# Kernel optimization log

Measured on AMD Instinct MI355X. Metric: run time of the kernel, lower is better.

Reference implementation:

```python
import jax, jax.numpy as jnp
import numpy as np

N, E_RAND, IN, HID, OUT = 10000, 320000, 512, 256, 256
E = E_RAND + N  # random edges + self loops
TEMP, LAM, LAMBDA_LOSS, BN_EPS = 0.5, 1e-3, 1.0, 1e-5


def _normalize(x):
    # F.normalize: x / max(||x||, 1e-12)
    return x / jnp.maximum(jnp.linalg.norm(x, axis=-1, keepdims=True), 1e-12)


def setup_inputs() -> dict:
    key = jax.random.key(0)
    ks = jax.random.split(key, 12)
    feat = jax.random.normal(ks[0], (N, IN), jnp.float32)
    loops = jnp.arange(N)
    src = jnp.concatenate([jax.random.randint(ks[1], (E_RAND,), 0, N), loops])
    dst = jnp.concatenate([jax.random.randint(ks[2], (E_RAND,), 0, N), loops])
    def lin(k, i, o):
        return jax.random.normal(k, (i, o), jnp.float32) / np.sqrt(i).astype(np.float32)
    return {
        'feat': feat,
        'W1': lin(ks[3], IN, HID), 'b1': jnp.zeros((HID,), jnp.float32),
        'W2': lin(ks[4], HID, OUT), 'b2': jnp.zeros((OUT,), jnp.float32),
        'Wt1': lin(ks[5], IN, HID), 'bt1': jnp.zeros((HID,), jnp.float32),
        'gamma': jnp.ones((HID,), jnp.float32), 'beta': jnp.zeros((HID,), jnp.float32),
        'Wt2': lin(ks[6], HID, OUT), 'bt2': jnp.zeros((OUT,), jnp.float32),
        'Wp': lin(ks[7], HID, HID), 'bp': jnp.zeros((HID,), jnp.float32),
        'src': src, 'dst': dst,
    }


def reference(feat, W1, b1, W2, b2, Wt1, bt1, gamma, beta, Wt2, bt2, Wp, bp, src, dst):
    n = feat.shape[0]
    ones = jnp.ones(src.shape, feat.dtype)
    deg_out = jax.ops.segment_sum(ones, src, num_segments=n)
    deg_in = jax.ops.segment_sum(ones, dst, num_segments=n)
    # symmetric GCN norm per edge (self-loops included so degrees >= 1)
    norm_e = jax.lax.rsqrt(deg_out)[src] * jax.lax.rsqrt(deg_in)[dst]

    def gconv(x, W, b):
        xw = x @ W  # [n, d_out]
        agg = jax.ops.segment_sum(xw[src] * norm_e[:, None], dst, num_segments=n)
        return agg + b

    # GCN encoder (2 layers, no LN)
    h = jax.nn.relu(gconv(feat, W1, b1))
    h = gconv(h, W2, b2)

    # target MLP encoder: linear -> BN(train) -> relu -> linear
    t = feat @ Wt1 + bt1
    mu = t.mean(0)
    var = t.var(0)  # biased, as BatchNorm normalization
    t = (t - mu) * jax.lax.rsqrt(var + BN_EPS) * gamma + beta
    trans = jax.nn.relu(t) @ Wt2 + bt2

    z = _normalize(h)                    # [n, d]
    q = _normalize(trans @ Wp + bp)      # projector (num_MLP=1)

    # pos_score: per-edge sum(z[u]*q[v])/temp, mean over in-edges at v
    sim_e = jnp.einsum('ed,ed->e', z[src], q[dst]) / TEMP
    pos = jax.ops.segment_sum(sim_e, dst, num_segments=n) / deg_in

    # neg_score (neg_sample=0): dense NxN similarity row-sums
    neg_sim = jnp.exp(z @ z.T / TEMP).sum(1)           # per-node
    neg_sim2 = LAM * jnp.exp(z @ q.T / TEMP).sum(1)    # per-node
    m_e = jnp.log(neg_sim[dst] + neg_sim2[src])
    neg = jax.ops.segment_sum(m_e, dst, num_segments=n) / deg_in

    loss = jnp.mean(-pos + LAMBDA_LOSS * neg)
    return loss
```

## Files before the change

kernel.cpp:

```cpp
#include <hip/hip_runtime.h>
#include <stdint.h>


#define TEMP_INV 2.0f
#define LAMC 1.0e-3f
#define SSCALE 1.6986436f

typedef __attribute__((ext_vector_type(8))) __bf16 bf16x8;
typedef __attribute__((ext_vector_type(8))) unsigned short u16x8;
typedef __attribute__((ext_vector_type(4))) float f32x4;

__device__ __forceinline__ unsigned short f2bf(float x) {
  union { float f; unsigned int u; } v; v.f = x;
  unsigned int r = v.u + 0x7FFFu + ((v.u >> 16) & 1u);
  return (unsigned short)(r >> 16);
}
__device__ __forceinline__ float bf2f(unsigned short h) {
  union { unsigned int u; float f; } v; v.u = ((unsigned int)h) << 16; return v.f;
}

__device__ __forceinline__ void g2lds16(const void* gc, void* l) {
  void* g = const_cast<void*>(gc);
  __builtin_amdgcn_global_load_lds(
      (__attribute__((address_space(1))) void*)g,
      (__attribute__((address_space(3))) void*)l, 16, 0, 0);
}

__global__ void k_deg(const int* __restrict__ src, const int* __restrict__ dst,
                      float* deg_out, float* deg_in, int E) {
  int i = blockIdx.x * blockDim.x + threadIdx.x;
  if (i < E) {
    atomicAdd(&deg_out[src[i]], 1.0f);
    atomicAdd(&deg_in[dst[i]], 1.0f);
  }
}

__global__ void k_rdeg(const float* __restrict__ deg_out, const float* __restrict__ deg_in,
                       float* rdo, float* rdi, float* idi, int N) {
  int i = blockIdx.x * blockDim.x + threadIdx.x;
  if (i < N) {
    float o = deg_out[i], d = deg_in[i];
    rdo[i] = rsqrtf(o);
    rdi[i] = rsqrtf(d);
    idi[i] = 1.0f / d;
  }
}

__global__ void k_scan(const float* __restrict__ deg, int* __restrict__ off, int N, int E) {
  __shared__ int sm[1024];
  int tid = threadIdx.x;
  int chunk = (N + 1023) / 1024;
  int b = tid * chunk;
  int sum = 0;
  for (int j = 0; j < chunk; j++) { int i = b + j; if (i < N) sum += (int)deg[i]; }
  sm[tid] = sum;
  __syncthreads();
  for (int s = 1; s < 1024; s <<= 1) {
    int v = (tid >= s) ? sm[tid - s] : 0;
    __syncthreads();
    sm[tid] += v;
    __syncthreads();
  }
  int run = (tid == 0) ? 0 : sm[tid - 1];
  for (int j = 0; j < chunk; j++) {
    int i = b + j;
    if (i < N) { off[i] = run; run += (int)deg[i]; }
  }
  if (tid == 0) off[N] = E;
}

__global__ void k_fill(const int* __restrict__ src, const int* __restrict__ dst,
                       const int* __restrict__ off, int* cur,
                       const float* __restrict__ rdo, const float* __restrict__ rdi,
                       int* adj, float* aw, int E) {
  int e = blockIdx.x * blockDim.x + threadIdx.x;
  if (e < E) {
    int u = src[e], v = dst[e];
    int slot = off[v] + atomicAdd(&cur[v], 1);
    adj[slot] = u;
    aw[slot] = rdo[u] * rdi[v];
  }
}

__global__ void k_cvtWt(const float* __restrict__ W, unsigned short* __restrict__ Wth,
                        unsigned short* __restrict__ Wtl, int K) {
  int k = blockIdx.x, c = threadIdx.x;
  float x = W[(size_t)k * 256 + c];
  unsigned short h = f2bf(x);
  Wth[(size_t)c * K + k] = h;
  Wtl[(size_t)c * K + k] = f2bf(x - bf2f(h));
}

template <int K, bool BIAS>
__global__ __launch_bounds__(256, 2) void k_gemmM(
    const float* A,
    const unsigned short* __restrict__ Wth, const unsigned short* __restrict__ Wtl,
    const float* __restrict__ bias, float* C, int M) {
  __shared__ __align__(1024) char LB[2][32768];
  const int tid = threadIdx.x, wv = tid >> 6, ln = tid & 63;
  const int rg = wv & 1, ch = wv >> 1;
  const int i0 = blockIdx.x * 32;
  int arow = i0 + rg * 16 + (ln & 15);
  if (arow >= M) arow = M - 1;
  const int kg = ln >> 4;
  const float* Ar = A + (size_t)arow * K + kg * 8;

  auto STAGE = [&](int kc, int b) {
#pragma unroll
    for (int it = 0; it < 8; it++) {
      int idx = it * 4 + wv;
      int mat = idx >> 4, s = (idx >> 2) & 3, cb = idx & 3;
      const unsigned short* Wt = mat ? Wtl : Wth;
      const char* src = (const char*)(Wt + (size_t)(cb * 64 + ln) * K) + kc * 64 + s * 16;
      g2lds16(src, (char*)LB[b] + mat * 16384 + s * 4096 + cb * 1024);
    }
  };

  auto LOADA = [&](int t, bf16x8& ah, bf16x8& al) {
    float4 x0 = *(const float4*)(Ar + t * 32);
    float4 x1 = *(const float4*)(Ar + t * 32 + 4);
    float xs[8] = {x0.x, x0.y, x0.z, x0.w, x1.x, x1.y, x1.z, x1.w};
    union { u16x8 u; bf16x8 b; } hu, lu;
#pragma unroll
    for (int j = 0; j < 8; j++) {
      unsigned short h = f2bf(xs[j]);
      hu.u[j] = h;
      lu.u[j] = f2bf(xs[j] - bf2f(h));
    }
    ah = hu.b; al = lu.b;
  };

  constexpr int NC = K / 32;
  STAGE(0, 0);
  bf16x8 ah, al;
  LOADA(0, ah, al);
  f32x4 acc[8] = {};
  int b = 0;
  __syncthreads();
  for (int t = 0; t < NC; t++) {
    bf16x8 ah_n = ah, al_n = al;
    if (t + 1 < NC) {
      STAGE(t + 1, b ^ 1);
      LOADA(t + 1, ah_n, al_n);
    }
    const char* Lb = (const char*)LB[b];
    __builtin_amdgcn_s_setprio(1);
#pragma unroll
    for (int jf = 0; jf < 8; jf++) {
      int col = ch * 128 + jf * 16 + (ln & 15);
      bf16x8 bh = *(const bf16x8*)(Lb + kg * 4096 + col * 16);
      bf16x8 bl = *(const bf16x8*)(Lb + 16384 + kg * 4096 + col * 16);
      acc[jf] = __builtin_amdgcn_mfma_f32_16x16x32_bf16(ah, bh, acc[jf], 0, 0, 0);
      acc[jf] = __builtin_amdgcn_mfma_f32_16x16x32_bf16(al, bh, acc[jf], 0, 0, 0);
      acc[jf] = __builtin_amdgcn_mfma_f32_16x16x32_bf16(ah, bl, acc[jf], 0, 0, 0);
    }
    __builtin_amdgcn_s_setprio(0);
    __syncthreads();
    b ^= 1; ah = ah_n; al = al_n;
  }
#pragma unroll
  for (int i = 0; i < 4; i++) {
    int row = i0 + rg * 16 + kg * 4 + i;
    if (row < M) {
#pragma unroll
      for (int jf = 0; jf < 8; jf++) {
        int col = ch * 128 + jf * 16 + (ln & 15);
        float v = acc[jf][i];
        if constexpr (BIAS) v += bias[col];
        C[(size_t)row * 256 + col] = v;
      }
    }
  }
}

__global__ void k_bnstat(const float* __restrict__ T, float* s, float* ss, int M) {
  int c = threadIdx.x;
  int r0 = blockIdx.x * 64;
  float a = 0, b = 0;
  for (int r = r0; r < r0 + 64 && r < M; r++) {
    float v = T[(size_t)r * 256 + c];
    a += v; b += v * v;
  }
  atomicAdd(&s[c], a);
  atomicAdd(&ss[c], b);
}

__global__ void k_bnrelu(float* T, const float* __restrict__ s, const float* __restrict__ ss,
                         const float* __restrict__ g, const float* __restrict__ b, int M) {
  int r = blockIdx.x, c = threadIdx.x;
  float invM = 1.0f / (float)M;
  float mu = s[c] * invM;
  float var = ss[c] * invM - mu * mu;
  float w = rsqrtf(var + 1e-5f) * g[c];
  float v = T[(size_t)r * 256 + c];
  v = (v - mu) * w + b[c];
  T[(size_t)r * 256 + c] = fmaxf(v, 0.0f);
}

template <bool UNIT, bool RELU>
__global__ __launch_bounds__(256) void k_aggS(
    const float* __restrict__ X, const int* __restrict__ off, const int* __restrict__ adj,
    const float* __restrict__ w, const float* __restrict__ bias, float* __restrict__ Y,
    int N, int NV) {
  int slice = blockIdx.x / NV, vc = blockIdx.x - slice * NV;
  int wv = threadIdx.x >> 6, ln = threadIdx.x & 63;
  int v = vc * 4 + wv;
  if (v >= N) return;
  int c = slice * 64 + ln;
  int s0 = off[v], s1 = off[v + 1];
  float acc = 0.f;
  int s = s0;
  for (; s + 3 < s1; s += 4) {
    int u0 = adj[s], u1 = adj[s + 1], u2 = adj[s + 2], u3 = adj[s + 3];
    float x0 = X[(size_t)u0 * 256 + c], x1 = X[(size_t)u1 * 256 + c];
    float x2 = X[(size_t)u2 * 256 + c], x3 = X[(size_t)u3 * 256 + c];
    if constexpr (UNIT) acc += (x0 + x1) + (x2 + x3);
    else acc += w[s] * x0 + w[s + 1] * x1 + w[s + 2] * x2 + w[s + 3] * x3;
  }
  for (; s < s1; s++) {
    float wt = UNIT ? 1.f : w[s];
    acc += wt * X[(size_t)adj[s] * 256 + c];
  }
  if constexpr (!UNIT) acc += bias[c];
  if constexpr (RELU) acc = fmaxf(acc, 0.f);
  Y[(size_t)v * 256 + c] = acc;
}

__global__ __launch_bounds__(256) void k_norm(float* X, unsigned short* Xb, int N, int NPAD) {
  int wv = threadIdx.x >> 6, ln = threadIdx.x & 63;
  int r = blockIdx.x * 4 + wv;
  if (r >= NPAD) return;
  if (r >= N) {
    ushort4 z = {0, 0, 0, 0};
    ((ushort4*)Xb)[(size_t)r * 64 + ln] = z;
    return;
  }
  float4 x = ((const float4*)X)[(size_t)r * 64 + ln];
  float ss = x.x * x.x + x.y * x.y + x.z * x.z + x.w * x.w;
#pragma unroll
  for (int m = 1; m < 64; m <<= 1) ss += __shfl_xor(ss, m, 64);
  float sc = 1.0f / fmaxf(sqrtf(ss), 1e-12f);
  float4 xn = {x.x * sc, x.y * sc, x.z * sc, x.w * sc};
  ((float4*)X)[(size_t)r * 64 + ln] = xn;
  float bs = sc * SSCALE;
  ushort4 b;
  b.x = f2bf(x.x * bs); b.y = f2bf(x.y * bs);
  b.z = f2bf(x.z * bs); b.w = f2bf(x.w * bs);
  ((ushort4*)Xb)[(size_t)r * 64 + ln] = b;
}

__global__ __launch_bounds__(256, 2) void k_sim(const unsigned short* __restrict__ Zb,
                                                const unsigned short* __restrict__ Qb,
                                                float* __restrict__ S1, float* __restrict__ S2,
                                                int N, int JT, int JS) {
  __shared__ __align__(1024) char LB[2][32768];
  const int tid = threadIdx.x;
  const int wv = tid >> 6, ln = tid & 63;
  const int i0 = blockIdx.x * 256;
  const int wb = wv * 64;

  auto STAGE = [&](int jt, int b) {
    int j0 = jt * 32;
    char* Lb = (char*)LB[b];
#pragma unroll
    for (int it = 0; it < 8; it++) {
      int c = it * 4 + wv;
      int L = c * 1024 + ln * 16;
      int r = L >> 9;
      int o = (L & 511) ^ ((r & 7) << 4);
      const char* g = (r < 32) ? (const char*)Zb + (size_t)(j0 + r) * 512 + o
                               : (const char*)Qb + (size_t)(j0 + r - 32) * 512 + o;
      g2lds16(g, Lb + c * 1024);
    }
  };

  int jt0 = (blockIdx.y * JT) / JS;
  int jt1 = ((blockIdx.y + 1) * JT) / JS;

  STAGE(jt0, 0);

  bf16x8 af[4][8];
#pragma unroll
  for (int rf = 0; rf < 4; rf++) {
    const char* arow = (const char*)(Zb + (size_t)(i0 + wb + rf * 16 + (ln & 15)) * 256);
#pragma unroll
    for (int kk = 0; kk < 8; kk++)
      af[rf][kk] = *(const bf16x8*)(arow + kk * 64 + ((ln >> 4) << 4));
  }

  f32x4 rs[4][2] = {};

  __syncthreads();
  int cur = 0;
  for (int jt = jt0; jt < jt1; jt++) {
    if (jt + 1 < jt1) STAGE(jt + 1, cur ^ 1);
    const char* Lb = (const char*)LB[cur];
#pragma unroll
    for (int m = 0; m < 2; m++) {
      f32x4 acc[4][2] = {};
      __builtin_amdgcn_s_setprio(1);
#pragma unroll
      for (int kk = 0; kk < 8; kk++) {
#pragma unroll
        for (int cf = 0; cf < 2; cf++) {
          int brow = m * 32 + cf * 16 + (ln & 15);
          int o = (kk * 64 + ((ln >> 4) << 4)) ^ ((brow & 7) << 4);
          bf16x8 bb = *(const bf16x8*)(Lb + brow * 512 + o);
#pragma unroll
          for (int rf = 0; rf < 4; rf++)
            acc[rf][cf] = __builtin_amdgcn_mfma_f32_16x16x32_bf16(af[rf][kk], bb, acc[rf][cf], 0, 0, 0);
        }
      }
      __builtin_amdgcn_s_setprio(0);
#pragma unroll
      for (int rf = 0; rf < 4; rf++)
#pragma unroll
        for (int i = 0; i < 4; i++)
          rs[rf][m][i] += exp2f(acc[rf][0][i]) + exp2f(acc[rf][1][i]);
    }
    __syncthreads();
    cur ^= 1;
  }

#pragma unroll
  for (int rf = 0; rf < 4; rf++)
#pragma unroll
    for (int m = 0; m < 2; m++)
#pragma unroll
      for (int i = 0; i < 4; i++) {
        float v = rs[rf][m][i];
        v += __shfl_xor(v, 1, 64);
        v += __shfl_xor(v, 2, 64);
        v += __shfl_xor(v, 4, 64);
        v += __shfl_xor(v, 8, 64);
        if ((ln & 15) == 0) {
          int row = i0 + wb + rf * 16 + ((ln >> 4) << 2) + i;
          if (row < N) atomicAdd(((m == 0) ? S1 : S2) + row, v);
        }
      }
}

__global__ __launch_bounds__(256) void k_final(const float* __restrict__ zsum, const float* __restrict__ q,
                                               const float* __restrict__ S1, const float* __restrict__ S2,
                                               const int* __restrict__ off, const int* __restrict__ adj,
                                               const float* __restrict__ idi, float* __restrict__ out,
                                               int N, float pad) {
  int wv = threadIdx.x >> 6, ln = threadIdx.x & 63;
  int v = blockIdx.x * 4 + wv;
  if (v >= N) return;
  float4 zs = ((const float4*)zsum)[(size_t)v * 64 + ln];
  float4 qv = ((const float4*)q)[(size_t)v * 64 + ln];
  float d = zs.x * qv.x + zs.y * qv.y + zs.z * qv.z + zs.w * qv.w;
  float s1v = S1[v] - pad;
  float lg = 0.0f;
  int e0 = off[v], e1 = off[v + 1];
  for (int s = e0 + ln; s < e1; s += 64) {
    int u = adj[s];
    lg += logf(s1v + LAMC * (S2[u] - pad));
  }
#pragma unroll
  for (int m = 1; m < 64; m <<= 1) {
    d += __shfl_xor(d, m, 64);
    lg += __shfl_xor(lg, m, 64);
  }
  if (ln == 0) {
    float inv = idi[v];
    float posv = d * inv * TEMP_INV;
    float negv = lg * inv;
    atomicAdd(out, (negv - posv) * (1.0f / (float)N));
  }
}

extern "C" void kernel_launch(void* const* d_in, const int* in_sizes, int n_in,
                              void* d_out, int out_size, void* d_ws, size_t ws_size,
                              hipStream_t stream) {
  const float* feat  = (const float*)d_in[0];
  const float* W1    = (const float*)d_in[1];
  const float* b1    = (const float*)d_in[2];
  const float* W2    = (const float*)d_in[3];
  const float* b2    = (const float*)d_in[4];
  const float* Wt1   = (const float*)d_in[5];
  const float* bt1   = (const float*)d_in[6];
  const float* gamma = (const float*)d_in[7];
  const float* beta  = (const float*)d_in[8];
  const float* Wt2   = (const float*)d_in[9];
  const float* bt2   = (const float*)d_in[10];
  const float* Wp    = (const float*)d_in[11];
  const float* bp    = (const float*)d_in[12];
  const int*   src   = (const int*)d_in[13];
  const int*   dst   = (const int*)d_in[14];
  const int N = in_sizes[0] / 512;
  const int E = in_sizes[13];
  const int NTI = (N + 255) / 256, NPAD = NTI * 256, JT = NPAD / 32;
  const int JS = 25;
  const float PADF = (float)(NPAD - N);

  char* p = (char*)d_ws;
  auto alloc = [&](size_t bytes) { char* r = p; p += (bytes + 255) & ~(size_t)255; return r; };
  float* B0 = (float*)alloc((size_t)N * 256 * 4);
  float* B1 = (float*)alloc((size_t)N * 256 * 4);
  float* B2 = (float*)alloc((size_t)N * 256 * 4);
  unsigned short* zb = (unsigned short*)alloc((size_t)NPAD * 256 * 2);
  unsigned short* qb = (unsigned short*)alloc((size_t)NPAD * 256 * 2);
  unsigned short* wth = (unsigned short*)alloc((size_t)256 * 512 * 2);
  unsigned short* wtl = (unsigned short*)alloc((size_t)256 * 512 * 2);
  int*   off = (int*)alloc((size_t)(N + 1) * 4);
  int*   adj = (int*)alloc((size_t)E * 4);
  float* aw  = (float*)alloc((size_t)E * 4);
  char*  zblk = p;
  float* deg_out = (float*)alloc((size_t)N * 4);
  float* deg_in  = (float*)alloc((size_t)N * 4);
  int*   cur     = (int*)alloc((size_t)N * 4);
  float* S1 = (float*)alloc((size_t)N * 4);
  float* S2 = (float*)alloc((size_t)N * 4);
  float* bns  = (float*)alloc(256 * 4);
  float* bnss = (float*)alloc(256 * 4);
  size_t zbytes = (size_t)(p - zblk);
  float* rdo = (float*)alloc((size_t)N * 4);
  float* rdi = (float*)alloc((size_t)N * 4);
  float* idi = (float*)alloc((size_t)N * 4);
  (void)ws_size; (void)n_in; (void)out_size;

  hipMemsetAsync(zblk, 0, zbytes, stream);
  hipMemsetAsync(d_out, 0, 4, stream);

  int gE = (E + 255) / 256, gN = (N + 255) / 256;
  int NV = (N + 3) / 4, gw = NV, gm = (N + 31) / 32;
  k_deg<<<gE, 256, 0, stream>>>(src, dst, deg_out, deg_in, E);
  k_rdeg<<<gN, 256, 0, stream>>>(deg_out, deg_in, rdo, rdi, idi, N);
  k_scan<<<1, 1024, 0, stream>>>(deg_in, off, N, E);
  k_fill<<<gE, 256, 0, stream>>>(src, dst, off, cur, rdo, rdi, adj, aw, E);

  k_cvtWt<<<512, 256, 0, stream>>>(W1, wth, wtl, 512);
  k_gemmM<512, false><<<gm, 256, 0, stream>>>(feat, wth, wtl, nullptr, B0, N);
  k_cvtWt<<<512, 256, 0, stream>>>(Wt1, wth, wtl, 512);
  k_gemmM<512, true ><<<gm, 256, 0, stream>>>(feat, wth, wtl, bt1, B1, N);

  k_bnstat<<<(N + 63) / 64, 256, 0, stream>>>(B1, bns, bnss, N);
  k_bnrelu<<<N, 256, 0, stream>>>(B1, bns, bnss, gamma, beta, N);

  k_cvtWt<<<256, 256, 0, stream>>>(Wt2, wth, wtl, 256);
  k_gemmM<256, true ><<<gm, 256, 0, stream>>>(B1, wth, wtl, bt2, B1, N);
  k_cvtWt<<<256, 256, 0, stream>>>(Wp, wth, wtl, 256);
  k_gemmM<256, true ><<<gm, 256, 0, stream>>>(B1, wth, wtl, bp, B1, N);

  k_aggS<false, true ><<<4 * gw, 256, 0, stream>>>(B0, off, adj, aw, b1, B2, N, NV);
  k_cvtWt<<<256, 256, 0, stream>>>(W2, wth, wtl, 256);
  k_gemmM<256, false><<<gm, 256, 0, stream>>>(B2, wth, wtl, nullptr, B0, N);
  k_aggS<false, false><<<4 * gw, 256, 0, stream>>>(B0, off, adj, aw, b2, B2, N, NV);

  int gnp = (NPAD + 3) / 4;
  k_norm<<<gnp, 256, 0, stream>>>(B2, zb, N, NPAD);
  k_norm<<<gnp, 256, 0, stream>>>(B1, qb, N, NPAD);

  dim3 gs(NTI, JS);
  k_sim<<<gs, 256, 0, stream>>>(zb, qb, S1, S2, N, JT, JS);

  k_aggS<true, false><<<4 * gw, 256, 0, stream>>>(B2, off, adj, aw, nullptr, B0, N, NV);
  k_final<<<gw, 256, 0, stream>>>(B0, B1, S1, S2, off, adj, idi, (float*)d_out, N, PADF);
}
```

Measured before the change: 781.6 us.

## Exploit z·zᵀ symmetry in similarity kernel and batch weight conversion and normalisation

The similarity kernel now computes the z·zᵀ exp block only for column tiles at or above the row block. Fully off-diagonal tiles also contribute column sums to S1 through atomics, which roughly halves the Z-Z MFMA and exp work. The exp2 scaling is replaced with __expf and a matching SSCALE, and the final log uses __logf. The five per-weight bf16 split conversion launches are merged into one LDS-tiled transposing kernel with separate buffers. The two normalisation launches are fused into one kernel. The cost is extra atomic traffic, some load imbalance between row blocks, and the lower accuracy of the fast math intrinsics.

```diff
diff --git a/kernel.cpp b/kernel.cpp
--- a/kernel.cpp
+++ b/kernel.cpp
@@ -4,7 +4,7 @@
 
 #define TEMP_INV 2.0f
 #define LAMC 1.0e-3f
-#define SSCALE 1.6986436f
+#define SSCALE 1.41421356f
 
 typedef __attribute__((ext_vector_type(8))) __bf16 bf16x8;
 typedef __attribute__((ext_vector_type(8))) unsigned short u16x8;
@@ -82,13 +82,33 @@
   }
 }
 
-__global__ void k_cvtWt(const float* __restrict__ W, unsigned short* __restrict__ Wth,
-                        unsigned short* __restrict__ Wtl, int K) {
-  int k = blockIdx.x, c = threadIdx.x;
-  float x = W[(size_t)k * 256 + c];
-  unsigned short h = f2bf(x);
-  Wth[(size_t)c * K + k] = h;
-  Wtl[(size_t)c * K + k] = f2bf(x - bf2f(h));
+__global__ __launch_bounds__(256) void k_cvtW5(
+    const float* __restrict__ Wa, const float* __restrict__ Wb, const float* __restrict__ Wc,
+    const float* __restrict__ Wd, const float* __restrict__ We,
+    unsigned short* Ha, unsigned short* Hb, unsigned short* Hc, unsigned short* Hd, unsigned short* He,
+    unsigned short* La, unsigned short* Lb, unsigned short* Lc, unsigned short* Ld, unsigned short* Le) {
+  int t = blockIdx.x;
+  const float* W; unsigned short* H; unsigned short* L; int K, loc;
+  if (t < 128)      { W = Wa; H = Ha; L = La; K = 512; loc = t; }
+  else if (t < 256) { W = Wb; H = Hb; L = Lb; K = 512; loc = t - 128; }
+  else if (t < 320) { W = Wc; H = Hc; L = Lc; K = 256; loc = t - 256; }
+  else if (t < 384) { W = Wd; H = Hd; L = Ld; K = 256; loc = t - 320; }
+  else              { W = We; H = He; L = Le; K = 256; loc = t - 384; }
+  int kt = loc >> 3, ct = loc & 7;
+  int k0 = kt * 32, c0 = ct * 32;
+  __shared__ float T[32][33];
+  int r = threadIdx.x >> 3, q = (threadIdx.x & 7) * 4;
+  float4 v = *(const float4*)(W + (size_t)(k0 + r) * 256 + c0 + q);
+  T[q + 0][r] = v.x; T[q + 1][r] = v.y; T[q + 2][r] = v.z; T[q + 3][r] = v.w;
+  __syncthreads();
+  float xs[4] = {T[r][q], T[r][q + 1], T[r][q + 2], T[r][q + 3]};
+  ushort4 h, l;
+  h.x = f2bf(xs[0]); l.x = f2bf(xs[0] - bf2f(h.x));
+  h.y = f2bf(xs[1]); l.y = f2bf(xs[1] - bf2f(h.y));
+  h.z = f2bf(xs[2]); l.z = f2bf(xs[2] - bf2f(h.z));
+  h.w = f2bf(xs[3]); l.w = f2bf(xs[3] - bf2f(h.w));
+  *(ushort4*)(H + (size_t)(c0 + r) * K + k0 + q) = h;
+  *(ushort4*)(L + (size_t)(c0 + r) * K + k0 + q) = l;
 }
 
 template <int K, bool BIAS>
@@ -226,27 +246,34 @@
   Y[(size_t)v * 256 + c] = acc;
 }
 
-__global__ __launch_bounds__(256) void k_norm(float* X, unsigned short* Xb, int N, int NPAD) {
+__global__ __launch_bounds__(256) void k_norm2(float* X0, unsigned short* Xb0,
+                                               float* X1, unsigned short* Xb1,
+                                               int N, int NPAD) {
   int wv = threadIdx.x >> 6, ln = threadIdx.x & 63;
   int r = blockIdx.x * 4 + wv;
   if (r >= NPAD) return;
-  if (r >= N) {
-    ushort4 z = {0, 0, 0, 0};
-    ((ushort4*)Xb)[(size_t)r * 64 + ln] = z;
-    return;
-  }
-  float4 x = ((const float4*)X)[(size_t)r * 64 + ln];
-  float ss = x.x * x.x + x.y * x.y + x.z * x.z + x.w * x.w;
-#pragma unroll
-  for (int m = 1; m < 64; m <<= 1) ss += __shfl_xor(ss, m, 64);
-  float sc = 1.0f / fmaxf(sqrtf(ss), 1e-12f);
-  float4 xn = {x.x * sc, x.y * sc, x.z * sc, x.w * sc};
-  ((float4*)X)[(size_t)r * 64 + ln] = xn;
-  float bs = sc * SSCALE;
-  ushort4 b;
-  b.x = f2bf(x.x * bs); b.y = f2bf(x.y * bs);
-  b.z = f2bf(x.z * bs); b.w = f2bf(x.w * bs);
-  ((ushort4*)Xb)[(size_t)r * 64 + ln] = b;
+#pragma unroll
+  for (int which = 0; which < 2; which++) {
+    float* X = which ? X1 : X0;
+    unsigned short* Xb = which ? Xb1 : Xb0;
+    if (r >= N) {
+      ushort4 z = {0, 0, 0, 0};
+      ((ushort4*)Xb)[(size_t)r * 64 + ln] = z;
+      continue;
+    }
+    float4 x = ((const float4*)X)[(size_t)r * 64 + ln];
+    float ss = x.x * x.x + x.y * x.y + x.z * x.z + x.w * x.w;
+#pragma unroll
+    for (int m = 1; m < 64; m <<= 1) ss += __shfl_xor(ss, m, 64);
+    float sc = 1.0f / fmaxf(sqrtf(ss), 1e-12f);
+    float4 xn = {x.x * sc, x.y * sc, x.z * sc, x.w * sc};
+    ((float4*)X)[(size_t)r * 64 + ln] = xn;
+    float bs = sc * SSCALE;
+    ushort4 b;
+    b.x = f2bf(x.x * bs); b.y = f2bf(x.y * bs);
+    b.z = f2bf(x.z * bs); b.w = f2bf(x.w * bs);
+    ((ushort4*)Xb)[(size_t)r * 64 + ln] = b;
+  }
 }
 
 __global__ __launch_bounds__(256, 2) void k_sim(const unsigned short* __restrict__ Zb,
@@ -259,11 +286,12 @@
   const int i0 = blockIdx.x * 256;
   const int wb = wv * 64;
 
-  auto STAGE = [&](int jt, int b) {
+  auto STAGE = [&](int jt, int b, bool qonly) {
     int j0 = jt * 32;
     char* Lb = (char*)LB[b];
 #pragma unroll
     for (int it = 0; it < 8; it++) {
+      if (qonly && it < 4) continue;
       int c = it * 4 + wv;
       int L = c * 1024 + ln * 16;
       int r = L >> 9;
@@ -277,7 +305,7 @@
   int jt0 = (blockIdx.y * JT) / JS;
   int jt1 = ((blockIdx.y + 1) * JT) / JS;
 
-  STAGE(jt0, 0);
+  STAGE(jt0, 0, jt0 * 32 < i0);
 
   bf16x8 af[4][8];
 #pragma unroll
@@ -293,17 +321,19 @@
   __syncthreads();
   int cur = 0;
   for (int jt = jt0; jt < jt1; jt++) {
-    if (jt + 1 < jt1) STAGE(jt + 1, cur ^ 1);
+    int j0 = jt * 32;
+    bool zyes = (j0 >= i0);
+    if (jt + 1 < jt1) STAGE(jt + 1, cur ^ 1, (jt + 1) * 32 < i0);
     const char* Lb = (const char*)LB[cur];
-#pragma unroll
-    for (int m = 0; m < 2; m++) {
+
+    if (zyes) {
       f32x4 acc[4][2] = {};
       __builtin_amdgcn_s_setprio(1);
 #pragma unroll
       for (int kk = 0; kk < 8; kk++) {
 #pragma unroll
         for (int cf = 0; cf < 2; cf++) {
-          int brow = m * 32 + cf * 16 + (ln & 15);
+          int brow = cf * 16 + (ln & 15);
           int o = (kk * 64 + ((ln >> 4) << 4)) ^ ((brow & 7) << 4);
           bf16x8 bb = *(const bf16x8*)(Lb + brow * 512 + o);
 #pragma unroll
@@ -312,12 +342,51 @@
         }
       }
       __builtin_amdgcn_s_setprio(0);
+      bool zfull = (j0 >= i0 + 256);
+      float cs0 = 0.f, cs1 = 0.f;
 #pragma unroll
       for (int rf = 0; rf < 4; rf++)
 #pragma unroll
+        for (int i = 0; i < 4; i++) {
+          float e0 = __expf(acc[rf][0][i]);
+          float e1 = __expf(acc[rf][1][i]);
+          rs[rf][0][i] += e0 + e1;
+          if (zfull) { cs0 += e0; cs1 += e1; }
+        }
+      if (zfull) {
+        cs0 += __shfl_xor(cs0, 16, 64); cs0 += __shfl_xor(cs0, 32, 64);
+        cs1 += __shfl_xor(cs1, 16, 64); cs1 += __shfl_xor(cs1, 32, 64);
+        if (ln < 16) {
+          int c0 = j0 + ln, c1 = j0 + 16 + ln;
+          if (c0 < N) atomicAdd(S1 + c0, cs0);
+          if (c1 < N) atomicAdd(S1 + c1, cs1);
+        }
+      }
+    }
+
+    {
+      f32x4 acc[4][2] = {};
+      __builtin_amdgcn_s_setprio(1);
+#pragma unroll
+      for (int kk = 0; kk < 8; kk++) {
+#pragma unroll
+        for (int cf = 0; cf < 2; cf++) {
+          int brow = 32 + cf * 16 + (ln & 15);
+          int o = (kk * 64 + ((ln >> 4) << 4)) ^ ((brow & 7) << 4);
+          bf16x8 bb = *(const bf16x8*)(Lb + brow * 512 + o);
+#pragma unroll
+          for (int rf = 0; rf < 4; rf++)
+            acc[rf][cf] = __builtin_amdgcn_mfma_f32_16x16x32_bf16(af[rf][kk], bb, acc[rf][cf], 0, 0, 0);
+        }
+      }
+      __builtin_amdgcn_s_setprio(0);
+#pragma unroll
+      for (int rf = 0; rf < 4; rf++)
+#pragma unroll
         for (int i = 0; i < 4; i++)
-          rs[rf][m][i] += exp2f(acc[rf][0][i]) + exp2f(acc[rf][1][i]);
-    }
+          rs[rf][1][i] += __expf(acc[rf][0][i]) + __expf(acc[rf][1][i]);
+    }
+
     __syncthreads();
     cur ^= 1;
   }
@@ -356,7 +425,7 @@
   int e0 = off[v], e1 = off[v + 1];
   for (int s = e0 + ln; s < e1; s += 64) {
     int u = adj[s];
-    lg += logf(s1v + LAMC * (S2[u] - pad));
+    lg += __logf(s1v + LAMC * (S2[u] - pad));
   }
 #pragma unroll
   for (int m = 1; m < 64; m <<= 1) {
@@ -402,8 +471,12 @@
   float* B2 = (float*)alloc((size_t)N * 256 * 4);
   unsigned short* zb = (unsigned short*)alloc((size_t)NPAD * 256 * 2);
   unsigned short* qb = (unsigned short*)alloc((size_t)NPAD * 256 * 2);
-  unsigned short* wth = (unsigned short*)alloc((size_t)256 * 512 * 2);
-  unsigned short* wtl = (unsigned short*)alloc((size_t)256 * 512 * 2);
+  unsigned short* wh[5]; unsigned short* wl[5];
+  const int KS[5] = {512, 512, 256, 256, 256};
+  for (int i = 0; i < 5; i++) {
+    wh[i] = (unsigned short*)alloc((size_t)256 * KS[i] * 2);
+    wl[i] = (unsigned short*)alloc((size_t)256 * KS[i] * 2);
+  }
   int*   off = (int*)alloc((size_t)(N + 1) * 4);
   int*   adj = (int*)alloc((size_t)E * 4);
   float* aw  = (float*)alloc((size_t)E * 4);
@@ -426,32 +499,31 @@
 
   int gE = (E + 255) / 256, gN = (N + 255) / 256;
   int NV = (N + 3) / 4, gw = NV, gm = (N + 31) / 32;
+
+  k_cvtW5<<<448, 256, 0, stream>>>(W1, Wt1, Wt2, Wp, W2,
+                                   wh[0], wh[1], wh[2], wh[3], wh[4],
+                                   wl[0], wl[1], wl[2], wl[3], wl[4]);
+
   k_deg<<<gE, 256, 0, stream>>>(src, dst, deg_out, deg_in, E);
   k_rdeg<<<gN, 256, 0, stream>>>(deg_out, deg_in, rdo, rdi, idi, N);
   k_scan<<<1, 1024, 0, stream>>>(deg_in, off, N, E);
   k_fill<<<gE, 256, 0, stream>>>(src, dst, off, cur, rdo, rdi, adj, aw, E);
 
-  k_cvtWt<<<512, 256, 0, stream>>>(W1, wth, wtl, 512);
-  k_gemmM<512, false><<<gm, 256, 0, stream>>>(feat, wth, wtl, nullptr, B0, N);
-  k_cvtWt<<<512, 256, 0, stream>>>(Wt1, wth, wtl, 512);
-  k_gemmM<512, true ><<<gm, 256, 0, stream>>>(feat, wth, wtl, bt1, B1, N);
+  k_gemmM<512, false><<<gm, 256, 0, stream>>>(feat, wh[0], wl[0], nullptr, B0, N);
+  k_gemmM<512, true ><<<gm, 256, 0, stream>>>(feat, wh[1], wl[1], bt1, B1, N);
 
   k_bnstat<<<(N + 63) / 64, 256, 0, stream>>>(B1, bns, bnss, N);
   k_bnrelu<<<N, 256, 0, stream>>>(B1, bns, bnss, gamma, beta, N);
 
-  k_cvtWt<<<256, 256, 0, stream>>>(Wt2, wth, wtl, 256);
-  k_gemmM<256, true ><<<gm, 256, 0, stream>>>(B1, wth, wtl, bt2, B1, N);
-  k_cvtWt<<<256, 256, 0, stream>>>(Wp, wth, wtl, 256);
-  k_gemmM<256, true ><<<gm, 256, 0, stream>>>(B1, wth, wtl, bp, B1, N);
+  k_gemmM<256, true ><<<gm, 256, 0, stream>>>(B1, wh[2], wl[2], bt2, B1, N);
+  k_gemmM<256, true ><<<gm, 256, 0, stream>>>(B1, wh[3], wl[3], bp, B1, N);
 
   k_aggS<false, true ><<<4 * gw, 256, 0, stream>>>(B0, off, adj, aw, b1, B2, N, NV);
-  k_cvtWt<<<256, 256, 0, stream>>>(W2, wth, wtl, 256);
-  k_gemmM<256, false><<<gm, 256, 0, stream>>>(B2, wth, wtl, nullptr, B0, N);
+  k_gemmM<256, false><<<gm, 256, 0, stream>>>(B2, wh[4], wl[4], nullptr, B0, N);
   k_aggS<false, false><<<4 * gw, 256, 0, stream>>>(B0, off, adj, aw, b2, B2, N, NV);
 
   int gnp = (NPAD + 3) / 4;
-  k_norm<<<gnp, 256, 0, stream>>>(B2, zb, N, NPAD);
-  k_norm<<<gnp, 256, 0, stream>>>(B1, qb, N, NPAD);
+  k_norm2<<<gnp, 256, 0, stream>>>(B2, zb, B1, qb, N, NPAD);
 
   dim3 gs(NTI, JS);
   k_sim<<<gs, 256, 0, stream>>>(zb, qb, S1, S2, N, JT, JS);
```

New measurement: 749.5 us. -4.1%, faster.
